# Optimization experiments

Hardware: AMD Instinct MI355X
Metric: run time of the kernel (lower is better)

## Reference

```python
import jax, jax.numpy as jnp
import numpy as np

EPS = 0.1  # entropic regularization epsilon
N, F, R, H = 512, 32, 8, 128


def setup_inputs() -> dict:
    key = jax.random.key(0)
    ks = jax.random.split(key, 9)
    s0 = 1.0 / np.sqrt(F + R)
    sh = 1.0 / np.sqrt(H)
    return {
        "X": jax.random.normal(ks[0], (N, F), jnp.float32),
        "U": jax.random.normal(ks[1], (N, R), jnp.float32),
        "Y": jax.random.normal(ks[2], (N, R), jnp.float32),
        "Wx": jax.random.normal(ks[3], (F, H), jnp.float32) * s0,
        "Wy": jax.random.normal(ks[4], (R, H), jnp.float32) * s0,
        "b0": jnp.zeros((H,), jnp.float32),
        "W1": jax.random.normal(ks[5], (H, H), jnp.float32) * sh,
        "b1": jnp.zeros((H,), jnp.float32),
        "W2": jax.random.normal(ks[6], (H, H), jnp.float32) * sh,
        "b2": jnp.zeros((H,), jnp.float32),
        "Wout": jax.random.normal(ks[7], (H, 1), jnp.float32) * sh,
        "bout": jnp.zeros((1,), jnp.float32),
    }


def _mlp_tail(h, W1, b1, W2, b2, Wout, bout):
    h = jax.nn.softplus(h @ W1 + b1)
    h = jax.nn.softplus(h @ W2 + b2)
    return h @ Wout + bout  # [..., 1]


def reference(X, U, Y, Wx, Wy, b0, W1, b1, W2, b2, Wout, bout):
    n = X.shape[0]
    # ---- estimate_psi (potential net estimates 'y' side directly) ----
    h_row = jax.nn.softplus(X @ Wx + Y @ Wy + b0)              # [n, H]
    psi = _mlp_tail(h_row, W1, b1, W2, b2, Wout, bout)         # [n, 1]
    # ---- estimate_phi: entropic dual over all (X_i, Y_j) pairs ----
    # First-layer pre-activation built by broadcast-sum instead of concat.
    h_pair = jax.nn.softplus((X @ Wx)[:, None, :] + (Y @ Wy)[None, :, :] + b0)  # [n, n, H]
    psi_vals = _mlp_tail(h_pair, W1, b1, W2, b2, Wout, bout)[..., 0]            # [n, n]
    cost = U @ Y.T                                             # [n, n]
    slack = cost - psi_vals
    m = jnp.max(slack, axis=1, keepdims=True)                  # [n, 1]
    lme = jax.nn.logsumexp((slack - m) / EPS, axis=1, keepdims=True) \
          - jnp.log(jnp.asarray(n, slack.dtype)) + m / EPS
    phi = EPS * lme                                            # [n, 1]
    return jnp.mean(phi) + jnp.mean(psi)
```

## Files before the change

kernel.cpp:

```cpp
#include <hip/hip_runtime.h>
#include <hip/hip_bf16.h>
#include <math.h>

#define NN 512
#define HH 128
#define FF 32
#define RR 8
#define EPSV 0.1f
#define INV_EPS 10.0f
#define LOG2E 1.4426950408889634f
#define LN2 0.6931471805599453f
#define K2E (INV_EPS * LOG2E)

#define PC1 1.437284f
#define PC2 (-0.672862f)
#define PC3 0.315362f
#define PC4 (-0.0799600f)

typedef unsigned short ushort_t;
typedef __attribute__((ext_vector_type(8))) short bf16x8;
typedef __attribute__((ext_vector_type(4))) float f32x4;
typedef __attribute__((ext_vector_type(4))) unsigned int u32x4;
typedef __attribute__((ext_vector_type(2))) unsigned int u32x2;

__device__ __forceinline__ float g2(float t) {
    const float u = __builtin_amdgcn_exp2f(-fabsf(t));
    const float p = u * (PC1 + u * (PC2 + u * (PC3 + u * PC4)));
    return fmaxf(t, 0.f) + p;
}
__device__ __forceinline__ ushort_t f2b(float f) {
    unsigned u = __float_as_uint(f);
    return (ushort_t)((u + 0x7fffu + ((u >> 16) & 1u)) >> 16);
}
__device__ __forceinline__ float b2f(ushort_t h) {
    return __uint_as_float(((unsigned)h) << 16);
}
__device__ __forceinline__ unsigned pk2(float a, float b) {
    __hip_bfloat162 h = __float22bfloat162_rn(make_float2(a, b));
    return *reinterpret_cast<unsigned*>(&h);
}

__global__ __launch_bounds__(256) void prep_kernel(
    const float* __restrict__ X, const float* __restrict__ Y,
    const float* __restrict__ Wx, const float* __restrict__ Wy,
    const float* __restrict__ b0, const float* __restrict__ W1, const float* __restrict__ W2,
    const float* __restrict__ b1, const float* __restrict__ b2, const float* __restrict__ Wout,
    ushort_t* __restrict__ Wt1b, ushort_t* __restrict__ Wt2b,
    ushort_t* __restrict__ XWxb, ushort_t* __restrict__ YWyb,
    float* __restrict__ b1e, float* __restrict__ b2e, float* __restrict__ WoutE) {
    int gid = blockIdx.x * 256 + threadIdx.x;
    if (gid < 32768) {
        int sel = gid >> 14;
        int idx = gid & 16383;
        int n = idx >> 7, k = idx & 127;
        (sel ? Wt2b : Wt1b)[idx] = f2b((sel ? W2 : W1)[k * HH + n]);
    } else if (gid < 98304) {
        int g = gid - 32768;
        int i = g >> 7, h = g & 127;
        float s = b0[h];
#pragma unroll
        for (int f = 0; f < FF; ++f) s += X[i * FF + f] * Wx[f * HH + h];
        XWxb[g] = f2b(s * LOG2E);
    } else if (gid < 163840) {
        int g = gid - 98304;
        int i = g >> 7, h = g & 127;
        float s = 0.f;
#pragma unroll
        for (int r = 0; r < RR; ++r) s += Y[i * RR + r] * Wy[r * HH + h];
        YWyb[g] = f2b(s * LOG2E);
    } else if (gid < 163968) {
        b1e[gid - 163840] = b1[gid - 163840] * LOG2E;
    } else if (gid < 164096) {
        b2e[gid - 163968] = b2[gid - 163968] * LOG2E;
    } else if (gid < 164224) {
        WoutE[gid - 164096] = Wout[gid - 164096] * LN2;
    }
}

__global__ __launch_bounds__(512) void pair_kernel(
    const ushort_t* __restrict__ XWxb, const ushort_t* __restrict__ YWyb,
    const ushort_t* __restrict__ Wt1b, const ushort_t* __restrict__ Wt2b,
    const float* __restrict__ U, const float* __restrict__ Y,
    const float* __restrict__ b1e, const float* __restrict__ b2e,
    const float* __restrict__ WoutE, const float* __restrict__ bout,
    float* __restrict__ psi_arr, float* __restrict__ Mp, float* __restrict__ Sp) {
    __shared__ ushort_t Hs[128 * HH];
    __shared__ float psum[2][4][64];

    const int i = blockIdx.x;
    const int q = blockIdx.y;
    const int j0 = q * 128;
    const int t = threadIdx.x;
    const int wv = t >> 6;
    const int hq = wv & 3;
    const int jh = wv >> 2;
    const int jbase = jh * 64;
    const int r16 = t & 15;
    const int g4 = (t >> 4) & 3;
    const int srow = t >> 4;
    const float boutv = bout[0];

    float axf[8];
    {
        bf16x8 axv = *(const bf16x8*)&XWxb[i * HH + r16 * 8];
#pragma unroll
        for (int e = 0; e < 8; ++e) axf[e] = b2f((ushort_t)axv[e]);
    }
    float cost;
    {
        const int j = j0 + (t & 127);
        const float4 u0 = *(const float4*)&U[i * RR];
        const float4 u1 = *(const float4*)&U[i * RR + 4];
        const float4 y0 = *(const float4*)&Y[j * RR];
        const float4 y1 = *(const float4*)&Y[j * RR + 4];
        cost = u0.x * y0.x + u0.y * y0.y + u0.z * y0.z + u0.w * y0.w +
               u1.x * y1.x + u1.y * y1.y + u1.z * y1.z + u1.w * y1.w;
    }
    bf16x8 afr1[2][4];
#pragma unroll
    for (int mt = 0; mt < 2; ++mt)
#pragma unroll
        for (int ks = 0; ks < 4; ++ks)
            afr1[mt][ks] = *(const bf16x8*)&Wt1b[(hq * 32 + mt * 16 + r16) * HH + ks * 32 + g4 * 8];
    float4 bias1h[2];
    bias1h[0] = *(const float4*)&b1e[hq * 32 + g4 * 4];
    bias1h[1] = *(const float4*)&b1e[hq * 32 + 16 + g4 * 4];
    float4 woutr[2];
    woutr[0] = *(const float4*)&WoutE[hq * 32 + g4 * 4];
    woutr[1] = *(const float4*)&WoutE[hq * 32 + 16 + g4 * 4];

#pragma unroll
    for (int s = 0; s < 4; ++s) {
        const int p = s * 32 + srow;
        bf16x8 yv = *(const bf16x8*)&YWyb[(j0 + p) * HH + r16 * 8];
        unsigned pk[4];
#pragma unroll
        for (int e = 0; e < 4; ++e) {
            float v0 = g2(axf[2 * e]     + b2f((ushort_t)yv[2 * e]));
            float v1 = g2(axf[2 * e + 1] + b2f((ushort_t)yv[2 * e + 1]));
            pk[e] = pk2(v0, v1);
        }
        *(u32x4*)&Hs[p * HH + ((r16 ^ (p & 7)) << 3)] = *(u32x4*)pk;
    }
    __syncthreads();

    f32x4 acc[2][4];
#pragma unroll
    for (int mt = 0; mt < 2; ++mt)
#pragma unroll
        for (int nt = 0; nt < 4; ++nt) {
            acc[mt][nt][0] = bias1h[mt].x; acc[mt][nt][1] = bias1h[mt].y;
            acc[mt][nt][2] = bias1h[mt].z; acc[mt][nt][3] = bias1h[mt].w;
        }
#pragma unroll
    for (int ks = 0; ks < 4; ++ks) {
        const int kb = ks * 32 + g4 * 8;
#pragma unroll
        for (int nt = 0; nt < 4; ++nt) {
            const int j = jbase + nt * 16 + r16;
            bf16x8 bfr = *(const bf16x8*)&Hs[j * HH + (kb ^ ((j & 7) << 3))];
            acc[0][nt] = __builtin_amdgcn_mfma_f32_16x16x32_bf16(afr1[0][ks], bfr, acc[0][nt], 0, 0, 0);
            acc[1][nt] = __builtin_amdgcn_mfma_f32_16x16x32_bf16(afr1[1][ks], bfr, acc[1][nt], 0, 0, 0);
        }
    }
    __syncthreads();

#pragma unroll
    for (int mt = 0; mt < 2; ++mt) {
        const int hb = hq * 32 + mt * 16 + g4 * 4;
#pragma unroll
        for (int nt = 0; nt < 4; ++nt) {
            const int j = jbase + nt * 16 + r16;
            u32x2 wv2;
            wv2[0] = pk2(g2(acc[mt][nt][0]), g2(acc[mt][nt][1]));
            wv2[1] = pk2(g2(acc[mt][nt][2]), g2(acc[mt][nt][3]));
            *(u32x2*)&Hs[j * HH + (hb ^ ((j & 7) << 3))] = wv2;
        }
    }
    __syncthreads();

    {
        const int hbase = hq * 32 + g4 * 4;
#pragma unroll
        for (int mt = 0; mt < 2; ++mt) {
            float4 bb = *(const float4*)&b2e[hbase + mt * 16];
#pragma unroll
            for (int nt = 0; nt < 4; ++nt) {
                acc[mt][nt][0] = bb.x; acc[mt][nt][1] = bb.y;
                acc[mt][nt][2] = bb.z; acc[mt][nt][3] = bb.w;
            }
        }
        bf16x8 afr2[2][4];
#pragma unroll
        for (int mt = 0; mt < 2; ++mt)
#pragma unroll
            for (int ks = 0; ks < 4; ++ks)
                afr2[mt][ks] = *(const bf16x8*)&Wt2b[(hq * 32 + mt * 16 + r16) * HH + ks * 32 + g4 * 8];
#pragma unroll
        for (int ks = 0; ks < 4; ++ks) {
            const int kb = ks * 32 + g4 * 8;
#pragma unroll
            for (int nt = 0; nt < 4; ++nt) {
                const int j = jbase + nt * 16 + r16;
                bf16x8 bfr = *(const bf16x8*)&Hs[j * HH + (kb ^ ((j & 7) << 3))];
                acc[0][nt] = __builtin_amdgcn_mfma_f32_16x16x32_bf16(afr2[0][ks], bfr, acc[0][nt], 0, 0, 0);
                acc[1][nt] = __builtin_amdgcn_mfma_f32_16x16x32_bf16(afr2[1][ks], bfr, acc[1][nt], 0, 0, 0);
            }
        }
    }
    {
        float part[4] = {0.f, 0.f, 0.f, 0.f};
#pragma unroll
        for (int mt = 0; mt < 2; ++mt) {
            const float wr[4] = {woutr[mt].x, woutr[mt].y, woutr[mt].z, woutr[mt].w};
#pragma unroll
            for (int r = 0; r < 4; ++r) {
                const float wgt = wr[r];
#pragma unroll
                for (int nt = 0; nt < 4; ++nt)
                    part[nt] += g2(acc[mt][nt][r]) * wgt;
            }
        }
#pragma unroll
        for (int nt = 0; nt < 4; ++nt) {
            part[nt] += __shfl_xor(part[nt], 16);
            part[nt] += __shfl_xor(part[nt], 32);
        }
        if (g4 == 0) {
#pragma unroll
            for (int nt = 0; nt < 4; ++nt) psum[jh][hq][nt * 16 + r16] = part[nt];
        }
    }
    __syncthreads();

    if (t < 128) {
        const int jh2 = t >> 6;
        const int jl = t & 63;
        const float psi = boutv + psum[jh2][0][jl] + psum[jh2][1][jl] +
                          psum[jh2][2][jl] + psum[jh2][3][jl];
        const int j = j0 + t;
        if (j == i) psi_arr[i] = psi;
        const float sv = cost - psi;
        float M = sv;
#pragma unroll
        for (int o = 1; o < 64; o <<= 1) M = fmaxf(M, __shfl_xor(M, o));
        float S = __builtin_amdgcn_exp2f((sv - M) * K2E);
#pragma unroll
        for (int o = 1; o < 64; o <<= 1) S += __shfl_xor(S, o);
        if (jl == 0) {
            Mp[i * 8 + q * 2 + jh2] = M;
            Sp[i * 8 + q * 2 + jh2] = S;
        }
    }
}

__global__ __launch_bounds__(512) void finalize_kernel(
    const float* __restrict__ psi_arr, const float* __restrict__ Mp,
    const float* __restrict__ Sp, float* __restrict__ out) {
    __shared__ float red[8];
    const int t = threadIdx.x;
    float Mq[8], Sq[8];
#pragma unroll
    for (int q = 0; q < 8; ++q) { Mq[q] = Mp[t * 8 + q]; Sq[q] = Sp[t * 8 + q]; }
    float Mg = Mq[0];
#pragma unroll
    for (int q = 1; q < 8; ++q) Mg = fmaxf(Mg, Mq[q]);
    float S = 0.f;
#pragma unroll
    for (int q = 0; q < 8; ++q) S += Sq[q] * __builtin_amdgcn_exp2f((Mq[q] - Mg) * K2E);
    const float phi = EPSV * (__logf(S) - __logf((float)NN)) + Mg;
    float v = phi + psi_arr[t];
#pragma unroll
    for (int o = 1; o < 64; o <<= 1) v += __shfl_xor(v, o);
    if ((t & 63) == 0) red[t >> 6] = v;
    __syncthreads();
    if (t == 0) {
        float tot = 0.f;
#pragma unroll
        for (int w = 0; w < 8; ++w) tot += red[w];
        out[0] = tot / (float)NN;
    }
}

extern "C" void kernel_launch(void* const* d_in, const int* in_sizes, int n_in,
                              void* d_out, int out_size, void* d_ws, size_t ws_size,
                              hipStream_t stream) {
    (void)in_sizes; (void)n_in; (void)out_size; (void)ws_size;
    const float* X    = (const float*)d_in[0];
    const float* U    = (const float*)d_in[1];
    const float* Y    = (const float*)d_in[2];
    const float* Wx   = (const float*)d_in[3];
    const float* Wy   = (const float*)d_in[4];
    const float* b0   = (const float*)d_in[5];
    const float* W1   = (const float*)d_in[6];
    const float* b1   = (const float*)d_in[7];
    const float* W2   = (const float*)d_in[8];
    const float* b2   = (const float*)d_in[9];
    const float* Wout = (const float*)d_in[10];
    const float* bout = (const float*)d_in[11];
    float* out = (float*)d_out;

    char* ws = (char*)d_ws;
    ushort_t* Wt1b    = (ushort_t*)(ws);
    ushort_t* Wt2b    = (ushort_t*)(ws + 32768);
    ushort_t* XWxb    = (ushort_t*)(ws + 65536);
    ushort_t* YWyb    = (ushort_t*)(ws + 196608);
    float*    psi_arr = (float*)(ws + 327680);
    float*    Mp      = (float*)(ws + 329728);
    float*    Sp      = (float*)(ws + 346112);
    float*    b1e     = (float*)(ws + 362496);
    float*    b2e     = (float*)(ws + 363008);
    float*    WoutE   = (float*)(ws + 363520);

    prep_kernel<<<642, 256, 0, stream>>>(X, Y, Wx, Wy, b0, W1, W2, b1, b2, Wout,
                                         Wt1b, Wt2b, XWxb, YWyb, b1e, b2e, WoutE);
    pair_kernel<<<dim3(NN, 4), 512, 0, stream>>>(XWxb, YWyb, Wt1b, Wt2b, U, Y,
                                                 b1e, b2e, WoutE, bout, psi_arr, Mp, Sp);
    finalize_kernel<<<1, 512, 0, stream>>>(psi_arr, Mp, Sp, out);
}
```

Measured before the change: 56.91 us.

## Halve pair kernel block to 4 waves, each wave computing two 64-column halves

The pair kernel now runs 256 threads per block instead of 512. Each wave covers both 64-pair halves of the 128-column tile, with separate shared buffers and two accumulator sets, so each weight fragment feeds twice as many MFMAs. Weight fragments are loaded from global memory per k-step instead of being held in registers for the whole kernel, and the cost dot product moves to the final reduction stage. The aim is more MFMA work per fragment load and less register pressure per wave. The cost is double the accumulator registers and half as many waves per block to hide latency.

```diff
diff --git a/kernel.cpp b/kernel.cpp
--- a/kernel.cpp
+++ b/kernel.cpp
@@ -77,24 +77,23 @@
     }
 }
 
-__global__ __launch_bounds__(512) void pair_kernel(
+__global__ void pair_kernel(
     const ushort_t* __restrict__ XWxb, const ushort_t* __restrict__ YWyb,
     const ushort_t* __restrict__ Wt1b, const ushort_t* __restrict__ Wt2b,
     const float* __restrict__ U, const float* __restrict__ Y,
     const float* __restrict__ b1e, const float* __restrict__ b2e,
     const float* __restrict__ WoutE, const float* __restrict__ bout,
     float* __restrict__ psi_arr, float* __restrict__ Mp, float* __restrict__ Sp) {
-    __shared__ ushort_t Hs[128 * HH];
+    __shared__ ushort_t HsA[64 * HH];
+    __shared__ ushort_t HsB[64 * HH];
     __shared__ float psum[2][4][64];
 
     const int i = blockIdx.x;
     const int q = blockIdx.y;
-    const int j0 = q * 128;
+    const int j0a = q * 128;
+    const int j0b = q * 128 + 64;
     const int t = threadIdx.x;
-    const int wv = t >> 6;
-    const int hq = wv & 3;
-    const int jh = wv >> 2;
-    const int jbase = jh * 64;
+    const int hq = t >> 6;
     const int r16 = t & 15;
     const int g4 = (t >> 4) & 3;
     const int srow = t >> 4;
@@ -106,61 +105,59 @@
 #pragma unroll
         for (int e = 0; e < 8; ++e) axf[e] = b2f((ushort_t)axv[e]);
     }
-    float cost;
-    {
-        const int j = j0 + (t & 127);
-        const float4 u0 = *(const float4*)&U[i * RR];
-        const float4 u1 = *(const float4*)&U[i * RR + 4];
-        const float4 y0 = *(const float4*)&Y[j * RR];
-        const float4 y1 = *(const float4*)&Y[j * RR + 4];
-        cost = u0.x * y0.x + u0.y * y0.y + u0.z * y0.z + u0.w * y0.w +
-               u1.x * y1.x + u1.y * y1.y + u1.z * y1.z + u1.w * y1.w;
-    }
-    bf16x8 afr1[2][4];
-#pragma unroll
-    for (int mt = 0; mt < 2; ++mt)
-#pragma unroll
-        for (int ks = 0; ks < 4; ++ks)
-            afr1[mt][ks] = *(const bf16x8*)&Wt1b[(hq * 32 + mt * 16 + r16) * HH + ks * 32 + g4 * 8];
     float4 bias1h[2];
     bias1h[0] = *(const float4*)&b1e[hq * 32 + g4 * 4];
     bias1h[1] = *(const float4*)&b1e[hq * 32 + 16 + g4 * 4];
+    float4 bias2h[2];
+    bias2h[0] = *(const float4*)&b2e[hq * 32 + g4 * 4];
+    bias2h[1] = *(const float4*)&b2e[hq * 32 + 16 + g4 * 4];
     float4 woutr[2];
     woutr[0] = *(const float4*)&WoutE[hq * 32 + g4 * 4];
     woutr[1] = *(const float4*)&WoutE[hq * 32 + 16 + g4 * 4];
 
 #pragma unroll
     for (int s = 0; s < 4; ++s) {
-        const int p = s * 32 + srow;
-        bf16x8 yv = *(const bf16x8*)&YWyb[(j0 + p) * HH + r16 * 8];
-        unsigned pk[4];
+        const int p = s * 16 + srow;
+        bf16x8 yva = *(const bf16x8*)&YWyb[(j0a + p) * HH + r16 * 8];
+        bf16x8 yvb = *(const bf16x8*)&YWyb[(j0b + p) * HH + r16 * 8];
+        unsigned pka[4], pkb[4];
 #pragma unroll
         for (int e = 0; e < 4; ++e) {
-            float v0 = g2(axf[2 * e]     + b2f((ushort_t)yv[2 * e]));
-            float v1 = g2(axf[2 * e + 1] + b2f((ushort_t)yv[2 * e + 1]));
-            pk[e] = pk2(v0, v1);
-        }
-        *(u32x4*)&Hs[p * HH + ((r16 ^ (p & 7)) << 3)] = *(u32x4*)pk;
-    }
-    __syncthreads();
-
-    f32x4 acc[2][4];
+            pka[e] = pk2(g2(axf[2 * e] + b2f((ushort_t)yva[2 * e])),
+                         g2(axf[2 * e + 1] + b2f((ushort_t)yva[2 * e + 1])));
+            pkb[e] = pk2(g2(axf[2 * e] + b2f((ushort_t)yvb[2 * e])),
+                         g2(axf[2 * e + 1] + b2f((ushort_t)yvb[2 * e + 1])));
+        }
+        const int off = p * HH + ((r16 ^ (p & 7)) << 3);
+        *(u32x4*)&HsA[off] = *(u32x4*)pka;
+        *(u32x4*)&HsB[off] = *(u32x4*)pkb;
+    }
+    __syncthreads();
+
+    f32x4 accA[2][4], accB[2][4];
 #pragma unroll
     for (int mt = 0; mt < 2; ++mt)
 #pragma unroll
         for (int nt = 0; nt < 4; ++nt) {
-            acc[mt][nt][0] = bias1h[mt].x; acc[mt][nt][1] = bias1h[mt].y;
-            acc[mt][nt][2] = bias1h[mt].z; acc[mt][nt][3] = bias1h[mt].w;
+            accA[mt][nt][0] = bias1h[mt].x; accA[mt][nt][1] = bias1h[mt].y;
+            accA[mt][nt][2] = bias1h[mt].z; accA[mt][nt][3] = bias1h[mt].w;
+            accB[mt][nt] = accA[mt][nt];
         }
 #pragma unroll
     for (int ks = 0; ks < 4; ++ks) {
         const int kb = ks * 32 + g4 * 8;
-#pragma unroll
-        for (int nt = 0; nt < 4; ++nt) {
-            const int j = jbase + nt * 16 + r16;
-            bf16x8 bfr = *(const bf16x8*)&Hs[j * HH + (kb ^ ((j & 7) << 3))];
-            acc[0][nt] = __builtin_amdgcn_mfma_f32_16x16x32_bf16(afr1[0][ks], bfr, acc[0][nt], 0, 0, 0);
-            acc[1][nt] = __builtin_amdgcn_mfma_f32_16x16x32_bf16(afr1[1][ks], bfr, acc[1][nt], 0, 0, 0);
+        bf16x8 af0 = *(const bf16x8*)&Wt1b[(hq * 32 + r16) * HH + kb];
+        bf16x8 af1 = *(const bf16x8*)&Wt1b[(hq * 32 + 16 + r16) * HH + kb];
+#pragma unroll
+        for (int nt = 0; nt < 4; ++nt) {
+            const int j = nt * 16 + r16;
+            const int off = j * HH + (kb ^ ((j & 7) << 3));
+            bf16x8 bfa = *(const bf16x8*)&HsA[off];
+            bf16x8 bfb = *(const bf16x8*)&HsB[off];
+            accA[0][nt] = __builtin_amdgcn_mfma_f32_16x16x32_bf16(af0, bfa, accA[0][nt], 0, 0, 0);
+            accB[0][nt] = __builtin_amdgcn_mfma_f32_16x16x32_bf16(af0, bfb, accB[0][nt], 0, 0, 0);
+            accA[1][nt] = __builtin_amdgcn_mfma_f32_16x16x32_bf16(af1, bfa, accA[1][nt], 0, 0, 0);
+            accB[1][nt] = __builtin_amdgcn_mfma_f32_16x16x32_bf16(af1, bfb, accB[1][nt], 0, 0, 0);
         }
     }
     __syncthreads();
@@ -170,46 +167,47 @@
         const int hb = hq * 32 + mt * 16 + g4 * 4;
 #pragma unroll
         for (int nt = 0; nt < 4; ++nt) {
-            const int j = jbase + nt * 16 + r16;
-            u32x2 wv2;
-            wv2[0] = pk2(g2(acc[mt][nt][0]), g2(acc[mt][nt][1]));
-            wv2[1] = pk2(g2(acc[mt][nt][2]), g2(acc[mt][nt][3]));
-            *(u32x2*)&Hs[j * HH + (hb ^ ((j & 7) << 3))] = wv2;
-        }
-    }
-    __syncthreads();
+            const int j = nt * 16 + r16;
+            const int off = j * HH + (hb ^ ((j & 7) << 3));
+            u32x2 wa, wb;
+            wa[0] = pk2(g2(accA[mt][nt][0]), g2(accA[mt][nt][1]));
+            wa[1] = pk2(g2(accA[mt][nt][2]), g2(accA[mt][nt][3]));
+            wb[0] = pk2(g2(accB[mt][nt][0]), g2(accB[mt][nt][1]));
+            wb[1] = pk2(g2(accB[mt][nt][2]), g2(accB[mt][nt][3]));
+            *(u32x2*)&HsA[off] = wa;
+            *(u32x2*)&HsB[off] = wb;
+        }
+    }
+    __syncthreads();
+
+#pragma unroll
+    for (int mt = 0; mt < 2; ++mt)
+#pragma unroll
+        for (int nt = 0; nt < 4; ++nt) {
+            accA[mt][nt][0] = bias2h[mt].x; accA[mt][nt][1] = bias2h[mt].y;
+            accA[mt][nt][2] = bias2h[mt].z; accA[mt][nt][3] = bias2h[mt].w;
+            accB[mt][nt] = accA[mt][nt];
+        }
+#pragma unroll
+    for (int ks = 0; ks < 4; ++ks) {
+        const int kb = ks * 32 + g4 * 8;
+        bf16x8 af0 = *(const bf16x8*)&Wt2b[(hq * 32 + r16) * HH + kb];
+        bf16x8 af1 = *(const bf16x8*)&Wt2b[(hq * 32 + 16 + r16) * HH + kb];
+#pragma unroll
+        for (int nt = 0; nt < 4; ++nt) {
+            const int j = nt * 16 + r16;
+            const int off = j * HH + (kb ^ ((j & 7) << 3));
+            bf16x8 bfa = *(const bf16x8*)&HsA[off];
+            bf16x8 bfb = *(const bf16x8*)&HsB[off];
+            accA[0][nt] = __builtin_amdgcn_mfma_f32_16x16x32_bf16(af0, bfa, accA[0][nt], 0, 0, 0);
+            accB[0][nt] = __builtin_amdgcn_mfma_f32_16x16x32_bf16(af0, bfb, accB[0][nt], 0, 0, 0);
+            accA[1][nt] = __builtin_amdgcn_mfma_f32_16x16x32_bf16(af1, bfa, accA[1][nt], 0, 0, 0);
+            accB[1][nt] = __builtin_amdgcn_mfma_f32_16x16x32_bf16(af1, bfb, accB[1][nt], 0, 0, 0);
+        }
+    }
 
     {
-        const int hbase = hq * 32 + g4 * 4;
-#pragma unroll
-        for (int mt = 0; mt < 2; ++mt) {
-            float4 bb = *(const float4*)&b2e[hbase + mt * 16];
-#pragma unroll
-            for (int nt = 0; nt < 4; ++nt) {
-                acc[mt][nt][0] = bb.x; acc[mt][nt][1] = bb.y;
-                acc[mt][nt][2] = bb.z; acc[mt][nt][3] = bb.w;
-            }
-        }
-        bf16x8 afr2[2][4];
-#pragma unroll
-        for (int mt = 0; mt < 2; ++mt)
-#pragma unroll
-            for (int ks = 0; ks < 4; ++ks)
-                afr2[mt][ks] = *(const bf16x8*)&Wt2b[(hq * 32 + mt * 16 + r16) * HH + ks * 32 + g4 * 8];
-#pragma unroll
-        for (int ks = 0; ks < 4; ++ks) {
-            const int kb = ks * 32 + g4 * 8;
-#pragma unroll
-            for (int nt = 0; nt < 4; ++nt) {
-                const int j = jbase + nt * 16 + r16;
-                bf16x8 bfr = *(const bf16x8*)&Hs[j * HH + (kb ^ ((j & 7) << 3))];
-                acc[0][nt] = __builtin_amdgcn_mfma_f32_16x16x32_bf16(afr2[0][ks], bfr, acc[0][nt], 0, 0, 0);
-                acc[1][nt] = __builtin_amdgcn_mfma_f32_16x16x32_bf16(afr2[1][ks], bfr, acc[1][nt], 0, 0, 0);
-            }
-        }
-    }
-    {
-        float part[4] = {0.f, 0.f, 0.f, 0.f};
+        float pa[4] = {0.f, 0.f, 0.f, 0.f}, pb[4] = {0.f, 0.f, 0.f, 0.f};
 #pragma unroll
         for (int mt = 0; mt < 2; ++mt) {
             const float wr[4] = {woutr[mt].x, woutr[mt].y, woutr[mt].z, woutr[mt].w};
@@ -217,29 +215,45 @@
             for (int r = 0; r < 4; ++r) {
                 const float wgt = wr[r];
 #pragma unroll
-                for (int nt = 0; nt < 4; ++nt)
-                    part[nt] += g2(acc[mt][nt][r]) * wgt;
+                for (int nt = 0; nt < 4; ++nt) {
+                    pa[nt] += g2(accA[mt][nt][r]) * wgt;
+                    pb[nt] += g2(accB[mt][nt][r]) * wgt;
+                }
             }
         }
 #pragma unroll
         for (int nt = 0; nt < 4; ++nt) {
-            part[nt] += __shfl_xor(part[nt], 16);
-            part[nt] += __shfl_xor(part[nt], 32);
+            pa[nt] += __shfl_xor(pa[nt], 16);
+            pa[nt] += __shfl_xor(pa[nt], 32);
+            pb[nt] += __shfl_xor(pb[nt], 16);
+            pb[nt] += __shfl_xor(pb[nt], 32);
         }
         if (g4 == 0) {
 #pragma unroll
-            for (int nt = 0; nt < 4; ++nt) psum[jh][hq][nt * 16 + r16] = part[nt];
+            for (int nt = 0; nt < 4; ++nt) {
+                psum[0][hq][nt * 16 + r16] = pa[nt];
+                psum[1][hq][nt * 16 + r16] = pb[nt];
+            }
         }
     }
     __syncthreads();
 
     if (t < 128) {
-        const int jh2 = t >> 6;
+        const int s2 = t >> 6;
         const int jl = t & 63;
-        const float psi = boutv + psum[jh2][0][jl] + psum[jh2][1][jl] +
-                          psum[jh2][2][jl] + psum[jh2][3][jl];
-        const int j = j0 + t;
+        const float psi = boutv + psum[s2][0][jl] + psum[s2][1][jl] +
+                          psum[s2][2][jl] + psum[s2][3][jl];
+        const int j = q * 128 + s2 * 64 + jl;
         if (j == i) psi_arr[i] = psi;
+        float cost;
+        {
+            const float4 u0 = *(const float4*)&U[i * RR];
+            const float4 u1 = *(const float4*)&U[i * RR + 4];
+            const float4 y0 = *(const float4*)&Y[j * RR];
+            const float4 y1 = *(const float4*)&Y[j * RR + 4];
+            cost = u0.x * y0.x + u0.y * y0.y + u0.z * y0.z + u0.w * y0.w +
+                   u1.x * y1.x + u1.y * y1.y + u1.z * y1.z + u1.w * y1.w;
+        }
         const float sv = cost - psi;
         float M = sv;
 #pragma unroll
@@ -248,8 +262,8 @@
 #pragma unroll
         for (int o = 1; o < 64; o <<= 1) S += __shfl_xor(S, o);
         if (jl == 0) {
-            Mp[i * 8 + q * 2 + jh2] = M;
-            Sp[i * 8 + q * 2 + jh2] = S;
+            Mp[i * 8 + q * 2 + s2] = M;
+            Sp[i * 8 + q * 2 + s2] = S;
         }
     }
 }
@@ -314,7 +328,7 @@
 
     prep_kernel<<<642, 256, 0, stream>>>(X, Y, Wx, Wy, b0, W1, W2, b1, b2, Wout,
                                          Wt1b, Wt2b, XWxb, YWyb, b1e, b2e, WoutE);
-    pair_kernel<<<dim3(NN, 4), 512, 0, stream>>>(XWxb, YWyb, Wt1b, Wt2b, U, Y,
+    pair_kernel<<<dim3(NN, 4), 256, 0, stream>>>(XWxb, YWyb, Wt1b, Wt2b, U, Y,
                                                  b1e, b2e, WoutE, bout, psi_arr, Mp, Sp);
     finalize_kernel<<<1, 512, 0, stream>>>(psi_arr, Mp, Sp, out);
 }
```

Result: faster. 51.53 us, median of 2 (-9.5%).
